# Kernel tuning notes

Measured on AMD Instinct MI355X. Metric: run time of the kernel, lower is better.

The kernel has to match this reference:

```python
import jax, jax.numpy as jnp
import numpy as np

SIZE = 4096
NB = 16            # nr_blocks_per_row
NDROP = 8          # nr_blocks_to_drop_per_row
BATCH = 8192
BLOCK = SIZE // NB # 256


def _block_mask():
    # latin_square(n): S[i,j] = ((i+j) mod n) + 1, values 1..n, each once per row/col
    i = np.arange(NB)
    S = ((i[:, None] + i[None, :]) % NB) + 1
    m = S > NDROP  # keep NB-NDROP blocks per row
    mask = np.repeat(np.repeat(m, BLOCK, axis=0), BLOCK, axis=1)
    return jnp.asarray(mask)  # [SIZE, SIZE] bool


def setup_inputs() -> dict:
    key = jax.random.key(0)
    kx, kw, kb = jax.random.split(key, 3)
    x = jax.random.normal(kx, (BATCH, SIZE), dtype=jnp.float32)
    # kaiming_normal_ default: fan_in mode, relu gain -> std = sqrt(2/fan_in)
    weight = jax.random.normal(kw, (SIZE, SIZE), dtype=jnp.float32) * jnp.sqrt(2.0 / SIZE)
    # uniform(-1,1) scaled by sqrt(1/size)
    bias = jax.random.uniform(kb, (SIZE,), minval=-1.0, maxval=1.0, dtype=jnp.float32) * jnp.sqrt(1.0 / SIZE)
    mask = _block_mask()
    return {"x": x, "weight": weight, "bias": bias, "mask": mask}


def reference(x, weight, bias, mask):
    # x @ (mask * weight).T + bias
    w = jnp.where(mask, weight, jnp.zeros((), dtype=weight.dtype))
    return x @ w.T + bias
```

## Files before the change

### kernel.cpp

```cpp
#include <hip/hip_runtime.h>
#include <hip/hip_bf16.h>
#include <stdint.h>


typedef __bf16 bf16x8 __attribute__((ext_vector_type(8)));
typedef float  f32x4  __attribute__((ext_vector_type(4)));

#define AS1 __attribute__((address_space(1)))
#define AS3 __attribute__((address_space(3)))

__device__ __forceinline__ void async_cp16(const void* g, void* l) {
  __builtin_amdgcn_global_load_lds((const AS1 void*)g, (AS3 void*)l, 16, 0, 0);
}

__device__ __forceinline__ uint32_t pack_bf16(float a, float b) {
  uint32_t ua = __float_as_uint(a);
  ua += 0x7fffu + ((ua >> 16) & 1u);
  uint32_t ub = __float_as_uint(b);
  ub += 0x7fffu + ((ub >> 16) & 1u);
  return (ua >> 16) | (ub & 0xffff0000u);
}

__global__ __launch_bounds__(256) void cvt_f32_bf16(const float* __restrict__ in,
                                                    uint32_t* __restrict__ out,
                                                    int n8) {
  int i = blockIdx.x * 256 + threadIdx.x;
  if (i >= n8) return;
  const float4* p = (const float4*)in + (size_t)i * 2;
  float4 a = p[0];
  float4 b = p[1];
  uint4 r;
  r.x = pack_bf16(a.x, a.y);
  r.y = pack_bf16(a.z, a.w);
  r.z = pack_bf16(b.x, b.y);
  r.w = pack_bf16(b.z, b.w);
  ((uint4*)out)[i] = r;
}

__global__ __launch_bounds__(256, 2) void gemm_bs(
    const uint16_t* __restrict__ X,
    const uint16_t* __restrict__ W,
    const float* __restrict__ bias,
    float* __restrict__ out) {
  constexpr int K = 4096;
  __shared__ uint16_t sA[128 * 32];
  __shared__ uint16_t sB[128 * 32];

  const int tid = threadIdx.x;
  const int bn = blockIdx.x;
  const int bm = blockIdx.y;
  const int m0 = bm << 7;
  const int n0 = bn << 7;
  const int bi = bn >> 1;

  const int tr = tid >> 2;
  const int tc = (tid & 3) << 3;
  const uint16_t* gA0 = X + (size_t)(m0 + tr) * K + tc;
  const uint16_t* gA1 = X + (size_t)(m0 + 64 + tr) * K + tc;
  const uint16_t* gB0 = W + (size_t)(n0 + tr) * K + tc;
  const uint16_t* gB1 = W + (size_t)(n0 + 64 + tr) * K + tc;
  uint16_t* lA0 = sA + tid * 8;
  uint16_t* lA1 = sA + 2048 + tid * 8;
  uint16_t* lB0 = sB + tid * 8;
  uint16_t* lB1 = sB + 2048 + tid * 8;

  const int lane = tid & 63;
  const int wv = tid >> 6;
  const int wm = (wv >> 1) << 6;
  const int wn = (wv & 1) << 6;
  const int fr = lane & 15;
  const int fk = (lane >> 4) << 3;

  f32x4 acc[4][4];
#pragma unroll
  for (int i = 0; i < 4; ++i)
#pragma unroll
    for (int j = 0; j < 4; ++j)
      acc[i][j] = (f32x4){0.f, 0.f, 0.f, 0.f};

  for (int t = 0; t < 8; ++t) {
    const int kb = ((24 + t - bi) & 15) << 8;
#pragma unroll
    for (int u = 0; u < 8; ++u) {
      const int kg = kb + (u << 5);
      __syncthreads();
      async_cp16(gA0 + kg, lA0);
      async_cp16(gA1 + kg, lA1);
      async_cp16(gB0 + kg, lB0);
      async_cp16(gB1 + kg, lB1);
      __syncthreads();

      bf16x8 av[4], bv[4];
#pragma unroll
      for (int i = 0; i < 4; ++i)
        av[i] = *(const bf16x8*)(sA + ((wm + (i << 4) + fr) << 5) + fk);
#pragma unroll
      for (int j = 0; j < 4; ++j)
        bv[j] = *(const bf16x8*)(sB + ((wn + (j << 4) + fr) << 5) + fk);
#pragma unroll
      for (int i = 0; i < 4; ++i)
#pragma unroll
        for (int j = 0; j < 4; ++j)
          acc[i][j] = __builtin_amdgcn_mfma_f32_16x16x32_bf16(av[i], bv[j],
                                                              acc[i][j], 0, 0, 0);
    }
  }

  const int rq = (lane >> 4) << 2;
#pragma unroll
  for (int j = 0; j < 4; ++j) {
    const int c = n0 + wn + (j << 4) + fr;
    const float bz = bias[c];
#pragma unroll
    for (int i = 0; i < 4; ++i) {
      const int r0 = m0 + wm + (i << 4) + rq;
#pragma unroll
      for (int r = 0; r < 4; ++r)
        out[(size_t)(r0 + r) * 4096 + c] = acc[i][j][r] + bz;
    }
  }
}

extern "C" void kernel_launch(void* const* d_in, const int* in_sizes, int n_in,
                              void* d_out, int out_size, void* d_ws, size_t ws_size,
                              hipStream_t stream) {
  const float* x = (const float*)d_in[0];
  const float* w = (const float*)d_in[1];
  const float* bias = (const float*)d_in[2];
  float* out = (float*)d_out;

  uint16_t* xb = (uint16_t*)d_ws;
  uint16_t* wb = xb + (size_t)8192 * 4096;

  const int nx8 = (8192 * 4096) / 8;
  const int nw8 = (4096 * 4096) / 8;
  hipLaunchKernelGGL(cvt_f32_bf16, dim3(nx8 / 256), dim3(256), 0, stream,
                     x, (uint32_t*)xb, nx8);
  hipLaunchKernelGGL(cvt_f32_bf16, dim3(nw8 / 256), dim3(256), 0, stream,
                     w, (uint32_t*)wb, nw8);

  dim3 grid(32, 64);
  hipLaunchKernelGGL(gemm_bs, grid, dim3(256), 0, stream, xb, wb, bias, out);
}
```

Baseline: 486.6 us.

## Pack only kept weight blocks, swizzle LDS reads, remap tile order

```diff
diff --git a/kernel.cpp b/kernel.cpp
--- a/kernel.cpp
+++ b/kernel.cpp
@@ -21,20 +21,33 @@
   return (ua >> 16) | (ub & 0xffff0000u);
 }
 
-__global__ __launch_bounds__(256) void cvt_f32_bf16(const float* __restrict__ in,
-                                                    uint32_t* __restrict__ out,
-                                                    int n8) {
-  int i = blockIdx.x * 256 + threadIdx.x;
-  if (i >= n8) return;
-  const float4* p = (const float4*)in + (size_t)i * 2;
-  float4 a = p[0];
-  float4 b = p[1];
-  uint4 r;
-  r.x = pack_bf16(a.x, a.y);
-  r.y = pack_bf16(a.z, a.w);
-  r.z = pack_bf16(b.x, b.y);
-  r.w = pack_bf16(b.z, b.w);
-  ((uint4*)out)[i] = r;
+__global__ __launch_bounds__(256) void cvt_x(const float* __restrict__ x,
+                                             uint2* __restrict__ xb) {
+  const int t = threadIdx.x;
+  const int b = blockIdx.x;
+  const float4* p = (const float4*)(x + (size_t)b * 4096);
+  uint2* o = xb + (size_t)b * 1024;
+  float4 a0 = p[t];
+  float4 a1 = p[t + 256];
+  float4 a2 = p[t + 512];
+  float4 a3 = p[t + 768];
+  o[t]       = make_uint2(pack_bf16(a0.x, a0.y), pack_bf16(a0.z, a0.w));
+  o[t + 256] = make_uint2(pack_bf16(a1.x, a1.y), pack_bf16(a1.z, a1.w));
+  o[t + 512] = make_uint2(pack_bf16(a2.x, a2.y), pack_bf16(a2.z, a2.w));
+  o[t + 768] = make_uint2(pack_bf16(a3.x, a3.y), pack_bf16(a3.z, a3.w));
+}
+
+__global__ __launch_bounds__(256) void cvt_w(const float* __restrict__ w,
+                                             uint2* __restrict__ wb) {
+  const int t = threadIdx.x;
+  const int n = blockIdx.x;
+  const int kstart = ((8 - (n >> 8)) & 15) << 8;
+  const float* src = w + (size_t)n * 4096;
+  uint2* dst = wb + (size_t)n * 512;
+  float4 a0 = *(const float4*)(src + ((kstart + 4 * t) & 4095));
+  float4 a1 = *(const float4*)(src + ((kstart + 1024 + 4 * t) & 4095));
+  dst[t]       = make_uint2(pack_bf16(a0.x, a0.y), pack_bf16(a0.z, a0.w));
+  dst[t + 256] = make_uint2(pack_bf16(a1.x, a1.y), pack_bf16(a1.z, a1.w));
 }
 
 __global__ __launch_bounds__(256, 2) void gemm_bs(
@@ -47,18 +60,20 @@
   __shared__ uint16_t sB[128 * 32];
 
   const int tid = threadIdx.x;
-  const int bn = blockIdx.x;
-  const int bm = blockIdx.y;
+  const int lin = blockIdx.x;
+  const int q = lin >> 3;
+  const int bn = ((lin & 7) << 2) + (q & 3);
+  const int bm = q >> 2;
   const int m0 = bm << 7;
   const int n0 = bn << 7;
   const int bi = bn >> 1;
 
   const int tr = tid >> 2;
-  const int tc = (tid & 3) << 3;
+  const int tc = (((tid & 3) ^ ((tr >> 1) & 3)) << 3);
   const uint16_t* gA0 = X + (size_t)(m0 + tr) * K + tc;
   const uint16_t* gA1 = X + (size_t)(m0 + 64 + tr) * K + tc;
-  const uint16_t* gB0 = W + (size_t)(n0 + tr) * K + tc;
-  const uint16_t* gB1 = W + (size_t)(n0 + 64 + tr) * K + tc;
+  const uint16_t* gB0 = W + (size_t)(n0 + tr) * 2048 + tc;
+  const uint16_t* gB1 = W + (size_t)(n0 + 64 + tr) * 2048 + tc;
   uint16_t* lA0 = sA + tid * 8;
   uint16_t* lA1 = sA + 2048 + tid * 8;
   uint16_t* lB0 = sB + tid * 8;
@@ -69,7 +84,7 @@
   const int wm = (wv >> 1) << 6;
   const int wn = (wv & 1) << 6;
   const int fr = lane & 15;
-  const int fk = (lane >> 4) << 3;
+  const int slotx = (((lane >> 4) ^ ((fr >> 1) & 3)) << 3);
 
   f32x4 acc[4][4];
 #pragma unroll
@@ -79,24 +94,26 @@
       acc[i][j] = (f32x4){0.f, 0.f, 0.f, 0.f};
 
   for (int t = 0; t < 8; ++t) {
-    const int kb = ((24 + t - bi) & 15) << 8;
+    const int kbA = ((24 + t - bi) & 15) << 8;
+    const int kbB = t << 8;
 #pragma unroll
     for (int u = 0; u < 8; ++u) {
-      const int kg = kb + (u << 5);
+      const int kA = kbA + (u << 5);
+      const int kB = kbB + (u << 5);
       __syncthreads();
-      async_cp16(gA0 + kg, lA0);
-      async_cp16(gA1 + kg, lA1);
-      async_cp16(gB0 + kg, lB0);
-      async_cp16(gB1 + kg, lB1);
+      async_cp16(gA0 + kA, lA0);
+      async_cp16(gA1 + kA, lA1);
+      async_cp16(gB0 + kB, lB0);
+      async_cp16(gB1 + kB, lB1);
       __syncthreads();
 
       bf16x8 av[4], bv[4];
 #pragma unroll
       for (int i = 0; i < 4; ++i)
-        av[i] = *(const bf16x8*)(sA + ((wm + (i << 4) + fr) << 5) + fk);
+        av[i] = *(const bf16x8*)(sA + ((wm + (i << 4) + fr) << 5) + slotx);
 #pragma unroll
       for (int j = 0; j < 4; ++j)
-        bv[j] = *(const bf16x8*)(sB + ((wn + (j << 4) + fr) << 5) + fk);
+        bv[j] = *(const bf16x8*)(sB + ((wn + (j << 4) + fr) << 5) + slotx);
 #pragma unroll
       for (int i = 0; i < 4; ++i)
 #pragma unroll
@@ -132,13 +149,9 @@
   uint16_t* xb = (uint16_t*)d_ws;
   uint16_t* wb = xb + (size_t)8192 * 4096;
 
-  const int nx8 = (8192 * 4096) / 8;
-  const int nw8 = (4096 * 4096) / 8;
-  hipLaunchKernelGGL(cvt_f32_bf16, dim3(nx8 / 256), dim3(256), 0, stream,
-                     x, (uint32_t*)xb, nx8);
-  hipLaunchKernelGGL(cvt_f32_bf16, dim3(nw8 / 256), dim3(256), 0, stream,
-                     w, (uint32_t*)wb, nw8);
+  hipLaunchKernelGGL(cvt_x, dim3(8192), dim3(256), 0, stream, x, (uint2*)xb);
+  hipLaunchKernelGGL(cvt_w, dim3(4096), dim3(256), 0, stream, w, (uint2*)wb);
 
-  dim3 grid(32, 64);
-  hipLaunchKernelGGL(gemm_bs, grid, dim3(256), 0, stream, xb, wb, bias, out);
+  hipLaunchKernelGGL(gemm_bs, dim3(2048), dim3(256), 0, stream,
+                     xb, wb, bias, out);
 }
```

Result: faster. 437.6 us (-10.1%).
